# Performance work log

Measured on AMD Instinct MI355X. Metric: run time of the kernel, lower is better.

Reference implementation:

```python
import jax, jax.numpy as jnp
import numpy as np

N = 50000      # n_nodes
E = 800000     # n_edges
IN_CH = 128
HID = 128
OUT_CH = 64
N_LAYERS = 4


def _linear_params(key, fan_in, fan_out):
    kw, kb = jax.random.split(key)
    bound = 1.0 / np.sqrt(fan_in)
    W = jax.random.uniform(kw, (fan_out, fan_in), jnp.float32, -bound, bound)
    b = jax.random.uniform(kb, (fan_out,), jnp.float32, -bound, bound)
    return W, b


def setup_inputs() -> dict:
    key = jax.random.key(0)
    ks = jax.random.split(key, 5)
    x = jax.random.normal(ks[0], (N, IN_CH), jnp.float32)
    edge_index = jax.random.randint(ks[1], (2, E), 0, N, dtype=jnp.int64)
    W_in, b_in = _linear_params(ks[2], IN_CH, HID)
    conv_keys = jax.random.split(ks[3], N_LAYERS)
    Wc = jnp.stack([_linear_params(k, HID, HID)[0] for k in conv_keys])
    bc = jnp.stack([_linear_params(k, HID, HID)[1] for k in conv_keys])
    W_out, b_out = _linear_params(ks[4], HID * N_LAYERS, OUT_CH)
    return {"x": x, "edge_index": edge_index, "W_in": W_in, "b_in": b_in,
            "Wc": Wc, "bc": bc, "W_out": W_out, "b_out": b_out}


def reference(x, edge_index, W_in, b_in, Wc, bc, W_out, b_out):
    n = x.shape[0]
    # input projection + relu
    x = jax.nn.relu(x @ W_in.T + b_in)
    src, dst = edge_index[0], edge_index[1]
    loop = jnp.arange(n, dtype=edge_index.dtype)
    src_a = jnp.concatenate([src, loop])   # [E+N]
    dst_a = jnp.concatenate([dst, loop])   # [E+N]
    # symmetric-normalized degree (with self loops)
    deg = jax.ops.segment_sum(jnp.ones(src_a.shape[0], x.dtype), dst_a, num_segments=n)
    norm = (deg[src_a] * deg[dst_a]) ** -0.5
    norm = jnp.where(jnp.isinf(norm), 0.0, norm)  # guard deg==0 (original sets inf->0)
    layer_outputs = []
    for i in range(Wc.shape[0]):
        h = x @ Wc[i].T + bc[i]                     # [N, HID]
        msg = h[src_a] * norm[:, None]              # gather + scale  [E+N, HID]
        out = jax.ops.segment_sum(msg, dst_a, num_segments=n)  # scatter-add
        x = jax.nn.relu(out)
        layer_outputs.append(x)
    h = jnp.concatenate(layer_outputs, axis=-1)     # jk_mode='cat' -> [N, HID*L]
    return h @ W_out.T + b_out
```

## Files before the change

kernel.cpp:

```cpp
#include <hip/hip_runtime.h>
#include <hip/hip_bf16.h>

#ifndef MIN
#define MIN(a,b) ((a)<(b)?(a):(b))
#endif

typedef _Float16 half2_t __attribute__((ext_vector_type(2)));
typedef _Float16 half4_t __attribute__((ext_vector_type(4)));
typedef _Float16 half8_t __attribute__((ext_vector_type(8)));
typedef float floatx4 __attribute__((ext_vector_type(4)));

#define BUCKET_SHIFT 6
#define BUCKET_SIZE 64
#define SCHUNK 2048


template <int BN, int KCH, bool A_F16, bool RELU, bool BIAS, bool SCALE, bool F16OUT>
__device__ __forceinline__
void gemm_body(int bid, const void* __restrict__ Av, int lda,
               const _Float16* __restrict__ W, int ldw,
               const float* __restrict__ bias, const float* __restrict__ dinv,
               void* __restrict__ Cv, int ldc, int M) {
    constexpr int NT = BN / 16;
    __shared__ __align__(16) _Float16 Ws[BN][136];

    int tid = threadIdx.x;
    int rowBase = bid * 64;
    int w = tid >> 6;
    int lane = tid & 63;
    int lrow = lane & 15;
    int quad = lane >> 4;
    int kq = quad * 8;
    int gr = rowBase + w * 16 + lrow;

    floatx4 acc[NT];
#pragma unroll
    for (int nt = 0; nt < NT; ++nt) acc[nt] = (floatx4){0.f, 0.f, 0.f, 0.f};

#pragma unroll
    for (int kc = 0; kc < KCH; ++kc) {
#pragma unroll
        for (int i = tid; i < BN * 16; i += 256) {
            int n = i >> 4, k8 = (i & 15) * 8;
            uint4 v = *(const uint4*)(W + (size_t)n * ldw + kc * 128 + k8);
            *(uint4*)(&Ws[n][k8]) = v;
        }
        __syncthreads();

        half8_t a[4];
        if (gr < M) {
            if (A_F16) {
                const _Float16* A = (const _Float16*)Av;
                const _Float16* ap = A + (size_t)gr * lda + kc * 128 + kq;
#pragma unroll
                for (int ks = 0; ks < 4; ++ks)
                    a[ks] = *(const half8_t*)(ap + ks * 32);
            } else {
                const float* A = (const float*)Av;
                const float* ap = A + (size_t)gr * lda + kc * 128 + kq;
#pragma unroll
                for (int ks = 0; ks < 4; ++ks) {
                    float4 v0 = *(const float4*)(ap + ks * 32);
                    float4 v1 = *(const float4*)(ap + ks * 32 + 4);
                    half8_t h;
                    h[0] = (_Float16)v0.x; h[1] = (_Float16)v0.y;
                    h[2] = (_Float16)v0.z; h[3] = (_Float16)v0.w;
                    h[4] = (_Float16)v1.x; h[5] = (_Float16)v1.y;
                    h[6] = (_Float16)v1.z; h[7] = (_Float16)v1.w;
                    a[ks] = h;
                }
            }
        } else {
#pragma unroll
            for (int ks = 0; ks < 4; ++ks)
                a[ks] = (half8_t){0, 0, 0, 0, 0, 0, 0, 0};
        }

#pragma unroll
        for (int ks = 0; ks < 4; ++ks) {
            int kk = ks * 32 + kq;
#pragma unroll
            for (int nt = 0; nt < NT; ++nt) {
                half8_t b = *(const half8_t*)(&Ws[nt * 16 + lrow][kk]);
                acc[nt] = __builtin_amdgcn_mfma_f32_16x16x32_f16(a[ks], b, acc[nt], 0, 0, 0);
            }
        }
        if (kc != KCH - 1) __syncthreads();
    }

#pragma unroll
    for (int nt = 0; nt < NT; ++nt) {
        int col = nt * 16 + lrow;
        float bv = BIAS ? bias[col] : 0.0f;
#pragma unroll
        for (int reg = 0; reg < 4; ++reg) {
            int gr2 = rowBase + w * 16 + quad * 4 + reg;
            if (gr2 < M) {
                float v = acc[nt][reg] + bv;
                if (RELU) v = fmaxf(v, 0.0f);
                if (SCALE) v *= dinv[gr2];
                if (F16OUT) {
                    _Float16* C = (_Float16*)Cv;
                    C[(size_t)gr2 * ldc + col] = (_Float16)v;
                } else {
                    float* C = (float*)Cv;
                    C[(size_t)gr2 * ldc + col] = v;
                }
            }
        }
    }
}

template <int BN, int KCH, bool A_F16, bool RELU, bool BIAS, bool SCALE, bool F16OUT>
__global__ __launch_bounds__(256)
void mfma_gemm(const void* __restrict__ Av, int lda,
               const _Float16* __restrict__ W, int ldw,
               const float* __restrict__ bias, const float* __restrict__ dinv,
               void* __restrict__ Cv, int ldc, int M) {
    gemm_body<BN, KCH, A_F16, RELU, BIAS, SCALE, F16OUT>(
        blockIdx.x, Av, lda, W, ldw, bias, dinv, Cv, ldc, M);
}


__global__ __launch_bounds__(256)
void k_hist_cvt(const int* __restrict__ dst, int E, int* __restrict__ bucketCnt, int NB,
                const float* __restrict__ a, _Float16* __restrict__ oa, int na,
                const float* __restrict__ b, _Float16* __restrict__ ob, int nb,
                const float* __restrict__ c, _Float16* __restrict__ oc, int nc,
                _Float16* __restrict__ zrow) {
    __shared__ int h[1024];
    int t = threadIdx.x;
    if (blockIdx.x < 512) {
        for (int i = t; i < 1024; i += 256) h[i] = 0;
        __syncthreads();
        for (int e = blockIdx.x * 256 + t; e < E; e += 512 * 256)
            atomicAdd(&h[dst[e] >> BUCKET_SHIFT], 1);
        __syncthreads();
        for (int i = t; i < NB; i += 256)
            if (h[i]) atomicAdd(&bucketCnt[i], h[i]);
    } else {
        int i = (blockIdx.x - 512) * 256 + t;
        if (i < na) oa[i] = (_Float16)a[i];
        if (i < nb) ob[i] = (_Float16)b[i];
        if (i < nc) oc[i] = (_Float16)c[i];
        if (i < 128) zrow[i] = (_Float16)0.0f;
    }
}

__global__ void bucket_scan(const int* __restrict__ bucketCnt,
                            int* __restrict__ bucketBase, int* __restrict__ bucketCur,
                            int NB, int E) {
    __shared__ int sm[1024];
    int t = threadIdx.x;
    int v = (t < NB) ? bucketCnt[t] : 0;
    sm[t] = v;
    __syncthreads();
    for (int off = 1; off < 1024; off <<= 1) {
        int add = (t >= off) ? sm[t - off] : 0;
        __syncthreads();
        sm[t] += add;
        __syncthreads();
    }
    if (t < NB) {
        bucketBase[t] = sm[t] - v;
        bucketCur[t] = sm[t] - v;
    }
    if (t == 0) bucketBase[NB] = E;
}


__global__ __launch_bounds__(256)
void k_scatter_proj(const int* __restrict__ src, const int* __restrict__ dst, int E,
                    int* __restrict__ bucketCur, unsigned int* __restrict__ rec, int SB,
                    const float* __restrict__ A, const _Float16* __restrict__ W,
                    const float* __restrict__ bias, _Float16* __restrict__ Cout, int M) {
    __shared__ int hist[1024];
    __shared__ int base[1024];
    if (blockIdx.x < SB) {
        int t = threadIdx.x;
        int e0 = blockIdx.x * SCHUNK;
        int e1 = MIN(E, e0 + SCHUNK);
        for (int i = t; i < 1024; i += 256) hist[i] = 0;
        __syncthreads();
        for (int e = e0 + t; e < e1; e += 256)
            atomicAdd(&hist[dst[e] >> BUCKET_SHIFT], 1);
        __syncthreads();
        for (int i = t; i < 1024; i += 256) {
            int c = hist[i];
            base[i] = c ? atomicAdd(&bucketCur[i], c) : 0;
            hist[i] = 0;
        }
        __syncthreads();
        for (int e = e0 + t; e < e1; e += 256) {
            int d = dst[e];
            int bk = d >> BUCKET_SHIFT;
            int pos = base[bk] + atomicAdd(&hist[bk], 1);
            rec[pos] = (unsigned)src[e] | ((unsigned)(d & (BUCKET_SIZE - 1)) << 16);
        }
    } else {
        gemm_body<128, 1, false, true, true, false, true>(
            blockIdx.x - SB, A, 128, W, 128, bias, nullptr, Cout, 128, M);
    }
}

__global__ void bucket_build(const unsigned int* __restrict__ rec,
                             const int* __restrict__ bucketBase,
                             int* __restrict__ rowptr, unsigned short* __restrict__ csr_src,
                             float* __restrict__ dinv, int N, int E) {
    __shared__ int lcnt[256];
    __shared__ int sm[256];
    __shared__ int lcur[64];
    int b = blockIdx.x;
    int t = threadIdx.x;
    int beg = bucketBase[b], end = bucketBase[b + 1];
    lcnt[t] = 0;
    __syncthreads();
    for (int i = beg + t; i < end; i += 256)
        atomicAdd(&lcnt[rec[i] >> 16], 1);
    __syncthreads();
    int v = lcnt[t];
    sm[t] = v;
    __syncthreads();
    for (int off = 1; off < 256; off <<= 1) {
        int add = (t >= off) ? sm[t - off] : 0;
        __syncthreads();
        sm[t] += add;
        __syncthreads();
    }
    int excl = sm[t] - v;
    if (t < BUCKET_SIZE) {
        int node = b * BUCKET_SIZE + t;
        if (node < N) {
            rowptr[node] = beg + excl;
            dinv[node] = rsqrtf((float)(v + 1));
        }
        lcur[t] = beg + excl;
    }
    __syncthreads();
    for (int i = beg + t; i < end; i += 256) {
        unsigned int r = rec[i];
        int pos = atomicAdd(&lcur[r >> 16], 1);
        csr_src[pos] = (unsigned short)(r & 0xFFFFu);
    }
    if (b == 0 && t == 0) rowptr[N] = E;
}


__global__ __launch_bounds__(256)
void agg_kernel(const half2_t* __restrict__ Hb, const float* __restrict__ dinv,
                const int* __restrict__ rowptr,
                const unsigned short* __restrict__ csr_src,
                half2_t* __restrict__ X, int N) {
    int node = blockIdx.x * 4 + (threadIdx.x >> 6);
    int t = threadIdx.x & 63;
    if (node >= N) return;
    float di = dinv[node];
    half2_t hu = Hb[(size_t)node * 64 + t];
    float2 acc;
    acc.x = (float)hu.x;
    acc.y = (float)hu.y;
    int beg = rowptr[node];
    int end = rowptr[node + 1];

    for (int base = beg; base < end; base += 64) {
        int idx = base + t;
        int s_lane = (idx < end) ? (int)csr_src[idx] : N;
        int m = end - base;
        if (m > 64) m = 64;
        int mm = (m + 15) & ~15;
        for (int j = 0; j < mm; j += 16) {
            int s[16];
#pragma unroll
            for (int k = 0; k < 16; ++k) s[k] = __shfl(s_lane, j + k);
            half2_t u[16];
#pragma unroll
            for (int k = 0; k < 16; ++k) u[k] = Hb[(size_t)s[k] * 64 + t];
#pragma unroll
            for (int k = 0; k < 16; ++k) {
                acc.x += (float)u[k].x;
                acc.y += (float)u[k].y;
            }
        }
    }
    half2_t o;
    o.x = (_Float16)fmaxf(acc.x * di, 0.0f);
    o.y = (_Float16)fmaxf(acc.y * di, 0.0f);
    X[(size_t)node * 256 + t] = o;
}


extern "C" void kernel_launch(void* const* d_in, const int* in_sizes, int n_in,
                              void* d_out, int out_size, void* d_ws, size_t ws_size,
                              hipStream_t stream) {
    const float* x     = (const float*)d_in[0];
    const int*   ei    = (const int*)d_in[1];
    const float* W_in  = (const float*)d_in[2];
    const float* b_in  = (const float*)d_in[3];
    const float* Wc    = (const float*)d_in[4];
    const float* bc    = (const float*)d_in[5];
    const float* W_out = (const float*)d_in[6];
    const float* b_out = (const float*)d_in[7];
    float* out = (float*)d_out;

    const int HID = 128;
    const int N = in_sizes[0] / HID;
    const int E = in_sizes[1] / 2;
    const int L = 4;
    const int* src = ei;
    const int* dst = ei + E;
    const int NB = (N + BUCKET_SIZE - 1) >> BUCKET_SHIFT;

    char* ws = (char*)d_ws;
    size_t off = 0;
    auto carve = [&](size_t bytes) {
        void* p = ws + off;
        off += (bytes + 255) & ~(size_t)255;
        return p;
    };
    float* dinv        = (float*)carve((size_t)N * 4);
    int*   rowptr      = (int*)carve((size_t)(N + 1) * 4);
    unsigned short* csr_src = (unsigned short*)carve((size_t)E * 2);
    unsigned int* rec  = (unsigned int*)carve((size_t)E * 4);
    int*   bucketCnt   = (int*)carve((size_t)1024 * 4);
    int*   bucketBase  = (int*)carve((size_t)1025 * 4);
    int*   bucketCur   = (int*)carve((size_t)1024 * 4);
    _Float16* bufA     = (_Float16*)carve((size_t)N * HID * 2);
    _Float16* bufH     = (_Float16*)carve((size_t)(N + 1) * HID * 2);
    _Float16* bufXcat  = (_Float16*)carve((size_t)N * 512 * 2);
    _Float16* Wf_in    = (_Float16*)carve((size_t)HID * HID * 2);
    _Float16* Wf_c     = (_Float16*)carve((size_t)L * HID * HID * 2);
    _Float16* Wf_out   = (_Float16*)carve((size_t)64 * 512 * 2);
    (void)ws_size;

    int gemm_blocks = (N + 63) / 64;
    int SB = (E + SCHUNK - 1) / SCHUNK;

    hipMemsetAsync(bucketCnt, 0, (size_t)1024 * 4, stream);
    k_hist_cvt<<<512 + 256, 256, 0, stream>>>(
        dst, E, bucketCnt, NB,
        W_in, Wf_in, HID * HID,
        Wc, Wf_c, L * HID * HID,
        W_out, Wf_out, 64 * 512,
        bufH + (size_t)N * HID);
    bucket_scan<<<1, 1024, 0, stream>>>(bucketCnt, bucketBase, bucketCur, NB, E);
    k_scatter_proj<<<SB + gemm_blocks, 256, 0, stream>>>(
        src, dst, E, bucketCur, rec, SB,
        x, Wf_in, b_in, bufA, N);
    bucket_build<<<NB, 256, 0, stream>>>(rec, bucketBase, rowptr, csr_src, dinv, N, E);

    for (int l = 0; l < L; ++l) {
        const void* Ain = (l == 0) ? (const void*)bufA
                                   : (const void*)(bufXcat + (size_t)(l - 1) * 128);
        int lda = (l == 0) ? 128 : 512;
        mfma_gemm<128, 1, true, false, true, true, true>
            <<<gemm_blocks, 256, 0, stream>>>(Ain, lda, Wf_c + (size_t)l * HID * HID, HID,
                                              bc + (size_t)l * HID, dinv, bufH, HID, N);
        agg_kernel<<<(N + 3) / 4, 256, 0, stream>>>((const half2_t*)bufH, dinv, rowptr,
                                                    csr_src,
                                                    (half2_t*)bufXcat + (size_t)l * 64, N);
    }

    mfma_gemm<64, 4, true, false, true, false, false>
        <<<gemm_blocks, 256, 0, stream>>>(bufXcat, 512, Wf_out, 512, b_out, nullptr,
                                          out, 64, N);
}
```

Before: 320.7 us.

## Gather neighbor rows with 16-byte loads across four lane groups in aggregation

The aggregation kernel now splits each 64-lane wavefront into four groups of 16 lanes. Each group loads a whole 256-byte neighbor row using uint4 (8 fp16) loads, so every iteration handles 16 neighbors with 4 wide loads per lane instead of 16 narrow half2 loads. Partial sums are combined across groups with xor shuffles, and one group writes the result with a single vector store. This cuts the number of load instructions and raises the bytes fetched per request, at the cost of more registers for accumulators and extra cross-lane reduction.

```diff
diff --git a/kernel.cpp b/kernel.cpp
--- a/kernel.cpp
+++ b/kernel.cpp
@@ -247,45 +247,69 @@
 
 
 __global__ __launch_bounds__(256)
-void agg_kernel(const half2_t* __restrict__ Hb, const float* __restrict__ dinv,
+void agg_kernel(const uint4* __restrict__ Hb4, const float* __restrict__ dinv,
                 const int* __restrict__ rowptr,
                 const unsigned short* __restrict__ csr_src,
-                half2_t* __restrict__ X, int N) {
+                _Float16* __restrict__ X, int N) {
     int node = blockIdx.x * 4 + (threadIdx.x >> 6);
     int t = threadIdx.x & 63;
     if (node >= N) return;
+    int g = t >> 4;
+    int c = t & 15;
     float di = dinv[node];
-    half2_t hu = Hb[(size_t)node * 64 + t];
-    float2 acc;
-    acc.x = (float)hu.x;
-    acc.y = (float)hu.y;
     int beg = rowptr[node];
     int end = rowptr[node + 1];
+
+    float acc[8] = {0.f, 0.f, 0.f, 0.f, 0.f, 0.f, 0.f, 0.f};
+
+    {
+        int selfs = (g == 0) ? node : N;
+        uint4 su = Hb4[(size_t)selfs * 16 + c];
+        half8_t h = *(const half8_t*)&su;
+#pragma unroll
+        for (int i = 0; i < 8; ++i) acc[i] += (float)h[i];
+    }
 
     for (int base = beg; base < end; base += 64) {
         int idx = base + t;
         int s_lane = (idx < end) ? (int)csr_src[idx] : N;
         int m = end - base;
         if (m > 64) m = 64;
-        int mm = (m + 15) & ~15;
-        for (int j = 0; j < mm; j += 16) {
-            int s[16];
-#pragma unroll
-            for (int k = 0; k < 16; ++k) s[k] = __shfl(s_lane, j + k);
-            half2_t u[16];
-#pragma unroll
-            for (int k = 0; k < 16; ++k) u[k] = Hb[(size_t)s[k] * 64 + t];
-#pragma unroll
-            for (int k = 0; k < 16; ++k) {
-                acc.x += (float)u[k].x;
-                acc.y += (float)u[k].y;
+        for (int j = 0; j < m; j += 16) {
+            int s0 = __shfl(s_lane, j + g);
+            int s1 = __shfl(s_lane, j + 4 + g);
+            int s2 = __shfl(s_lane, j + 8 + g);
+            int s3 = __shfl(s_lane, j + 12 + g);
+            uint4 u0 = Hb4[(size_t)s0 * 16 + c];
+            uint4 u1 = Hb4[(size_t)s1 * 16 + c];
+            uint4 u2 = Hb4[(size_t)s2 * 16 + c];
+            uint4 u3 = Hb4[(size_t)s3 * 16 + c];
+            half8_t h0 = *(const half8_t*)&u0;
+            half8_t h1 = *(const half8_t*)&u1;
+            half8_t h2 = *(const half8_t*)&u2;
+            half8_t h3 = *(const half8_t*)&u3;
+#pragma unroll
+            for (int i = 0; i < 8; ++i) {
+                acc[i] += (float)h0[i];
+                acc[i] += (float)h1[i];
+                acc[i] += (float)h2[i];
+                acc[i] += (float)h3[i];
             }
         }
     }
-    half2_t o;
-    o.x = (_Float16)fmaxf(acc.x * di, 0.0f);
-    o.y = (_Float16)fmaxf(acc.y * di, 0.0f);
-    X[(size_t)node * 256 + t] = o;
+
+#pragma unroll
+    for (int i = 0; i < 8; ++i) {
+        acc[i] += __shfl_xor(acc[i], 16);
+        acc[i] += __shfl_xor(acc[i], 32);
+    }
+
+    if (g == 0) {
+        half8_t o;
+#pragma unroll
+        for (int i = 0; i < 8; ++i) o[i] = (_Float16)fmaxf(acc[i] * di, 0.0f);
+        *(half8_t*)(X + (size_t)node * 512 + c * 8) = o;
+    }
 }
 
 
@@ -355,9 +379,9 @@
         mfma_gemm<128, 1, true, false, true, true, true>
             <<<gemm_blocks, 256, 0, stream>>>(Ain, lda, Wf_c + (size_t)l * HID * HID, HID,
                                               bc + (size_t)l * HID, dinv, bufH, HID, N);
-        agg_kernel<<<(N + 3) / 4, 256, 0, stream>>>((const half2_t*)bufH, dinv, rowptr,
+        agg_kernel<<<(N + 3) / 4, 256, 0, stream>>>((const uint4*)bufH, dinv, rowptr,
                                                     csr_src,
-                                                    (half2_t*)bufXcat + (size_t)l * 64, N);
+                                                    bufXcat + (size_t)l * 128, N);
     }
 
     mfma_gemm<64, 4, true, false, true, false, false>
```

After: 323.1 us. About the same (+0.7%).

## Split CSR into source-residue segments and aggregate several nodes per wave

Applied to the files above, without the earlier changes.

The CSR build now sorts each destination's edges into 4 sub-segments keyed by the low two bits of the source index, and stores a per-(node, segment) row pointer. The aggregation kernel gives each wave 7 consecutive nodes and walks all nodes segment by segment, using a fixed grid of 2048 blocks and gather batches of 8 instead of 16. The intent is better temporal locality of the feature gathers across the waves running at the same time. In exchange, each node's short edge list is cut into smaller pieces that are padded to 8, which adds wasted loads of the zero row. There are also fewer waves in flight and more serial work per wave.

```diff
diff --git a/kernel.cpp b/kernel.cpp
--- a/kernel.cpp
+++ b/kernel.cpp
@@ -13,6 +13,9 @@
 #define BUCKET_SHIFT 6
 #define BUCKET_SIZE 64
 #define SCHUNK 2048
+#define NSEG 4
+#define SEGMASK 3
+#define NPW 7
 
 
 template <int BN, int KCH, bool A_F16, bool RELU, bool BIAS, bool SCALE, bool F16OUT>
@@ -203,20 +206,23 @@
     }
 }
 
+
 __global__ void bucket_build(const unsigned int* __restrict__ rec,
                              const int* __restrict__ bucketBase,
-                             int* __restrict__ rowptr, unsigned short* __restrict__ csr_src,
+                             int* __restrict__ rowptr2, unsigned short* __restrict__ csr_src,
                              float* __restrict__ dinv, int N, int E) {
     __shared__ int lcnt[256];
     __shared__ int sm[256];
-    __shared__ int lcur[64];
+    __shared__ int lcur[256];
     int b = blockIdx.x;
     int t = threadIdx.x;
     int beg = bucketBase[b], end = bucketBase[b + 1];
     lcnt[t] = 0;
     __syncthreads();
-    for (int i = beg + t; i < end; i += 256)
-        atomicAdd(&lcnt[rec[i] >> 16], 1);
+    for (int i = beg + t; i < end; i += 256) {
+        unsigned int r = rec[i];
+        atomicAdd(&lcnt[((r >> 16) & 63) * NSEG + (r & SEGMASK)], 1);
+    }
     __syncthreads();
     int v = lcnt[t];
     sm[t] = v;
@@ -228,64 +234,99 @@
         __syncthreads();
     }
     int excl = sm[t] - v;
+    rowptr2[b * 256 + t] = beg + excl;
+    lcur[t] = beg + excl;
     if (t < BUCKET_SIZE) {
         int node = b * BUCKET_SIZE + t;
         if (node < N) {
-            rowptr[node] = beg + excl;
-            dinv[node] = rsqrtf((float)(v + 1));
-        }
-        lcur[t] = beg + excl;
+            int deg = lcnt[t * 4] + lcnt[t * 4 + 1] + lcnt[t * 4 + 2] + lcnt[t * 4 + 3];
+            dinv[node] = rsqrtf((float)(deg + 1));
+        }
     }
     __syncthreads();
     for (int i = beg + t; i < end; i += 256) {
         unsigned int r = rec[i];
-        int pos = atomicAdd(&lcur[r >> 16], 1);
+        int pos = atomicAdd(&lcur[((r >> 16) & 63) * NSEG + (r & SEGMASK)], 1);
         csr_src[pos] = (unsigned short)(r & 0xFFFFu);
     }
-    if (b == 0 && t == 0) rowptr[N] = E;
+    if (b == 0 && t == 0) rowptr2[gridDim.x * 256] = E;
 }
 
 
 __global__ __launch_bounds__(256)
 void agg_kernel(const half2_t* __restrict__ Hb, const float* __restrict__ dinv,
-                const int* __restrict__ rowptr,
+                const int* __restrict__ rowptr2,
                 const unsigned short* __restrict__ csr_src,
                 half2_t* __restrict__ X, int N) {
-    int node = blockIdx.x * 4 + (threadIdx.x >> 6);
+    int wid = blockIdx.x * 4 + (threadIdx.x >> 6);
     int t = threadIdx.x & 63;
-    if (node >= N) return;
-    float di = dinv[node];
-    half2_t hu = Hb[(size_t)node * 64 + t];
-    float2 acc;
-    acc.x = (float)hu.x;
-    acc.y = (float)hu.y;
-    int beg = rowptr[node];
-    int end = rowptr[node + 1];
-
-    for (int base = beg; base < end; base += 64) {
-        int idx = base + t;
-        int s_lane = (idx < end) ? (int)csr_src[idx] : N;
-        int m = end - base;
-        if (m > 64) m = 64;
-        int mm = (m + 15) & ~15;
-        for (int j = 0; j < mm; j += 16) {
-            int s[16];
-#pragma unroll
-            for (int k = 0; k < 16; ++k) s[k] = __shfl(s_lane, j + k);
-            half2_t u[16];
-#pragma unroll
-            for (int k = 0; k < 16; ++k) u[k] = Hb[(size_t)s[k] * 64 + t];
-#pragma unroll
-            for (int k = 0; k < 16; ++k) {
-                acc.x += (float)u[k].x;
-                acc.y += (float)u[k].y;
+    int n0 = wid * NPW;
+
+    float2 acc[NPW];
+    float di[NPW];
+#pragma unroll
+    for (int n = 0; n < NPW; ++n) {
+        int node = n0 + n;
+        if (node < N) {
+            di[n] = dinv[node];
+            half2_t hu = Hb[(size_t)node * 64 + t];
+            acc[n].x = (float)hu.x;
+            acc[n].y = (float)hu.y;
+        } else {
+            di[n] = 0.0f;
+            acc[n].x = 0.0f;
+            acc[n].y = 0.0f;
+        }
+    }
+
+    for (int s = 0; s < NSEG; ++s) {
+#pragma unroll
+        for (int n = 0; n < NPW; ++n) {
+            int node = n0 + n;
+            if (node >= N) continue;
+            int beg = rowptr2[node * NSEG + s];
+            int end = rowptr2[node * NSEG + s + 1];
+            for (int base = beg; base < end; base += 64) {
+                int idx = base + t;
+                int s_lane = (idx < end) ? (int)csr_src[idx] : N;
+                int m = end - base;
+                if (m > 64) m = 64;
+                int mm = (m + 7) & ~7;
+                for (int j = 0; j < mm; j += 8) {
+                    int s0 = __shfl(s_lane, j + 0), s1 = __shfl(s_lane, j + 1);
+                    int s2 = __shfl(s_lane, j + 2), s3 = __shfl(s_lane, j + 3);
+                    int s4 = __shfl(s_lane, j + 4), s5 = __shfl(s_lane, j + 5);
+                    int s6 = __shfl(s_lane, j + 6), s7 = __shfl(s_lane, j + 7);
+                    half2_t u0 = Hb[(size_t)s0 * 64 + t];
+                    half2_t u1 = Hb[(size_t)s1 * 64 + t];
+                    half2_t u2 = Hb[(size_t)s2 * 64 + t];
+                    half2_t u3 = Hb[(size_t)s3 * 64 + t];
+                    half2_t u4 = Hb[(size_t)s4 * 64 + t];
+                    half2_t u5 = Hb[(size_t)s5 * 64 + t];
+                    half2_t u6 = Hb[(size_t)s6 * 64 + t];
+                    half2_t u7 = Hb[(size_t)s7 * 64 + t];
+                    acc[n].x += (float)u0.x; acc[n].y += (float)u0.y;
+                    acc[n].x += (float)u1.x; acc[n].y += (float)u1.y;
+                    acc[n].x += (float)u2.x; acc[n].y += (float)u2.y;
+                    acc[n].x += (float)u3.x; acc[n].y += (float)u3.y;
+                    acc[n].x += (float)u4.x; acc[n].y += (float)u4.y;
+                    acc[n].x += (float)u5.x; acc[n].y += (float)u5.y;
+                    acc[n].x += (float)u6.x; acc[n].y += (float)u6.y;
+                    acc[n].x += (float)u7.x; acc[n].y += (float)u7.y;
+                }
             }
         }
     }
-    half2_t o;
-    o.x = (_Float16)fmaxf(acc.x * di, 0.0f);
-    o.y = (_Float16)fmaxf(acc.y * di, 0.0f);
-    X[(size_t)node * 256 + t] = o;
+
+#pragma unroll
+    for (int n = 0; n < NPW; ++n) {
+        int node = n0 + n;
+        if (node >= N) continue;
+        half2_t o;
+        o.x = (_Float16)fmaxf(acc[n].x * di[n], 0.0f);
+        o.y = (_Float16)fmaxf(acc[n].y * di[n], 0.0f);
+        X[(size_t)node * 256 + t] = o;
+    }
 }
 
 
@@ -318,7 +359,7 @@
         return p;
     };
     float* dinv        = (float*)carve((size_t)N * 4);
-    int*   rowptr      = (int*)carve((size_t)(N + 1) * 4);
+    int*   rowptr2     = (int*)carve(((size_t)NB * 256 + 8) * 4);
     unsigned short* csr_src = (unsigned short*)carve((size_t)E * 2);
     unsigned int* rec  = (unsigned int*)carve((size_t)E * 4);
     int*   bucketCnt   = (int*)carve((size_t)1024 * 4);
@@ -334,6 +375,7 @@
 
     int gemm_blocks = (N + 63) / 64;
     int SB = (E + SCHUNK - 1) / SCHUNK;
+    int agg_blocks = 2048;
 
     hipMemsetAsync(bucketCnt, 0, (size_t)1024 * 4, stream);
     k_hist_cvt<<<512 + 256, 256, 0, stream>>>(
@@ -346,7 +388,7 @@
     k_scatter_proj<<<SB + gemm_blocks, 256, 0, stream>>>(
         src, dst, E, bucketCur, rec, SB,
         x, Wf_in, b_in, bufA, N);
-    bucket_build<<<NB, 256, 0, stream>>>(rec, bucketBase, rowptr, csr_src, dinv, N, E);
+    bucket_build<<<NB, 256, 0, stream>>>(rec, bucketBase, rowptr2, csr_src, dinv, N, E);
 
     for (int l = 0; l < L; ++l) {
         const void* Ain = (l == 0) ? (const void*)bufA
@@ -355,9 +397,9 @@
         mfma_gemm<128, 1, true, false, true, true, true>
             <<<gemm_blocks, 256, 0, stream>>>(Ain, lda, Wf_c + (size_t)l * HID * HID, HID,
                                               bc + (size_t)l * HID, dinv, bufH, HID, N);
-        agg_kernel<<<(N + 3) / 4, 256, 0, stream>>>((const half2_t*)bufH, dinv, rowptr,
-                                                    csr_src,
-                                                    (half2_t*)bufXcat + (size_t)l * 64, N);
+        agg_kernel<<<agg_blocks, 256, 0, stream>>>((const half2_t*)bufH, dinv, rowptr2,
+                                                   csr_src,
+                                                   (half2_t*)bufXcat + (size_t)l * 64, N);
     }
 
     mfma_gemm<64, 4, true, false, true, false, false>
```

Measured after the change: 386.4 us. +20.5%, slower.

## Fuse neighbor aggregation with following layer GEMM and output projection

Applied to the files above, without the earlier changes.

Each layer's gather-aggregation is merged with the next layer's 128x128 MFMA projection in one kernel. The aggregated rows are staged in LDS as the GEMM A operand, with ping-pong H buffers between layers. The final layer's aggregation is fused into the output projection, so layer 4 is never written to Xcat and the earlier slabs are read from global memory. This removes four kernel launches and one round-trip of layer outputs, but cuts parallelism from 12.5k blocks of 4 nodes to about 782 blocks of 64 nodes, so each wave aggregates 16 nodes serially and the gather loses latency hiding.

```diff
diff --git a/kernel.cpp b/kernel.cpp
--- a/kernel.cpp
+++ b/kernel.cpp
@@ -122,12 +122,198 @@
 }
 
 
+__device__ __forceinline__
+float2 agg_node(const half2_t* __restrict__ Hin, const int* __restrict__ rowptr,
+                const unsigned short* __restrict__ csr_src, int node, int lane, int N) {
+    half2_t hu = Hin[(size_t)node * 64 + lane];
+    float2 acc;
+    acc.x = (float)hu.x;
+    acc.y = (float)hu.y;
+    int beg = rowptr[node];
+    int end = rowptr[node + 1];
+    for (int base = beg; base < end; base += 64) {
+        int idx = base + lane;
+        int s_lane = (idx < end) ? (int)csr_src[idx] : N;
+        int m = end - base;
+        if (m > 64) m = 64;
+        int mm = (m + 15) & ~15;
+        for (int j = 0; j < mm; j += 16) {
+            int s[16];
+#pragma unroll
+            for (int k = 0; k < 16; ++k) s[k] = __shfl(s_lane, j + k);
+            half2_t u[16];
+#pragma unroll
+            for (int k = 0; k < 16; ++k) u[k] = Hin[(size_t)s[k] * 64 + lane];
+#pragma unroll
+            for (int k = 0; k < 16; ++k) {
+                acc.x += (float)u[k].x;
+                acc.y += (float)u[k].y;
+            }
+        }
+    }
+    return acc;
+}
+
+
+__global__ __launch_bounds__(256)
+void fused_agg_conv(const half2_t* __restrict__ Hin, const float* __restrict__ dinv,
+                    const int* __restrict__ rowptr,
+                    const unsigned short* __restrict__ csr_src,
+                    half2_t* __restrict__ Xslab,
+                    const _Float16* __restrict__ W,
+                    const float* __restrict__ bias,
+                    _Float16* __restrict__ Hout, int N) {
+    __shared__ __align__(16) _Float16 As[64][136];
+    __shared__ __align__(16) _Float16 Ws[128][136];
+    int tid = threadIdx.x;
+    int w = tid >> 6;
+    int lane = tid & 63;
+    int rowBase = blockIdx.x * 64;
+
+#pragma unroll
+    for (int i = tid; i < 128 * 16; i += 256) {
+        int n = i >> 4, k8 = (i & 15) * 8;
+        *(uint4*)(&Ws[n][k8]) = *(const uint4*)(W + (size_t)n * 128 + k8);
+    }
+
+    for (int nn = 0; nn < 16; ++nn) {
+        int node = rowBase + w * 16 + nn;
+        half2_t o = {(_Float16)0.0f, (_Float16)0.0f};
+        if (node < N) {
+            float di = dinv[node];
+            float2 acc = agg_node(Hin, rowptr, csr_src, node, lane, N);
+            o.x = (_Float16)fmaxf(acc.x * di, 0.0f);
+            o.y = (_Float16)fmaxf(acc.y * di, 0.0f);
+            Xslab[(size_t)node * 256 + lane] = o;
+        }
+        *(half2_t*)(&As[w * 16 + nn][lane * 2]) = o;
+    }
+    __syncthreads();
+
+    int lrow = lane & 15;
+    int quad = lane >> 4;
+    int kq = quad * 8;
+    floatx4 acc[8];
+#pragma unroll
+    for (int nt = 0; nt < 8; ++nt) acc[nt] = (floatx4){0.f, 0.f, 0.f, 0.f};
+#pragma unroll
+    for (int ks = 0; ks < 4; ++ks) {
+        int kk = ks * 32 + kq;
+        half8_t a = *(const half8_t*)(&As[w * 16 + lrow][kk]);
+#pragma unroll
+        for (int nt = 0; nt < 8; ++nt) {
+            half8_t b = *(const half8_t*)(&Ws[nt * 16 + lrow][kk]);
+            acc[nt] = __builtin_amdgcn_mfma_f32_16x16x32_f16(a, b, acc[nt], 0, 0, 0);
+        }
+    }
+#pragma unroll
+    for (int nt = 0; nt < 8; ++nt) {
+        int col = nt * 16 + lrow;
+        float bv = bias[col];
+#pragma unroll
+        for (int reg = 0; reg < 4; ++reg) {
+            int gr2 = rowBase + w * 16 + quad * 4 + reg;
+            if (gr2 < N) {
+                float v = (acc[nt][reg] + bv) * dinv[gr2];
+                Hout[(size_t)gr2 * 128 + col] = (_Float16)v;
+            }
+        }
+    }
+}
+
+
+__global__ __launch_bounds__(256)
+void fused_agg_out(const half2_t* __restrict__ Hin, const float* __restrict__ dinv,
+                   const int* __restrict__ rowptr,
+                   const unsigned short* __restrict__ csr_src,
+                   const _Float16* __restrict__ Xcat,
+                   const _Float16* __restrict__ W,
+                   const float* __restrict__ bias, float* __restrict__ out, int N) {
+    __shared__ __align__(16) _Float16 As[64][136];
+    __shared__ __align__(16) _Float16 Ws[64][136];
+    int tid = threadIdx.x;
+    int w = tid >> 6;
+    int lane = tid & 63;
+    int rowBase = blockIdx.x * 64;
+
+    for (int nn = 0; nn < 16; ++nn) {
+        int node = rowBase + w * 16 + nn;
+        half2_t o = {(_Float16)0.0f, (_Float16)0.0f};
+        if (node < N) {
+            float di = dinv[node];
+            float2 acc = agg_node(Hin, rowptr, csr_src, node, lane, N);
+            o.x = (_Float16)fmaxf(acc.x * di, 0.0f);
+            o.y = (_Float16)fmaxf(acc.y * di, 0.0f);
+        }
+        *(half2_t*)(&As[w * 16 + nn][lane * 2]) = o;
+    }
+
+    int lrow = lane & 15;
+    int quad = lane >> 4;
+    int kq = quad * 8;
+    int gr = rowBase + w * 16 + lrow;
+
+    floatx4 acc[4];
+#pragma unroll
+    for (int nt = 0; nt < 4; ++nt) acc[nt] = (floatx4){0.f, 0.f, 0.f, 0.f};
+
+#pragma unroll
+    for (int kc = 0; kc < 4; ++kc) {
+        __syncthreads();
+#pragma unroll
+        for (int i = tid; i < 64 * 16; i += 256) {
+            int n = i >> 4, k8 = (i & 15) * 8;
+            *(uint4*)(&Ws[n][k8]) = *(const uint4*)(W + (size_t)n * 512 + kc * 128 + k8);
+        }
+        __syncthreads();
+
+        half8_t a[4];
+        if (kc == 3) {
+#pragma unroll
+            for (int ks = 0; ks < 4; ++ks)
+                a[ks] = *(const half8_t*)(&As[w * 16 + lrow][ks * 32 + kq]);
+        } else if (gr < N) {
+            const _Float16* ap = Xcat + (size_t)gr * 512 + kc * 128 + kq;
+#pragma unroll
+            for (int ks = 0; ks < 4; ++ks)
+                a[ks] = *(const half8_t*)(ap + ks * 32);
+        } else {
+#pragma unroll
+            for (int ks = 0; ks < 4; ++ks)
+                a[ks] = (half8_t){0, 0, 0, 0, 0, 0, 0, 0};
+        }
+
+#pragma unroll
+        for (int ks = 0; ks < 4; ++ks) {
+            int kk = ks * 32 + kq;
+#pragma unroll
+            for (int nt = 0; nt < 4; ++nt) {
+                half8_t b = *(const half8_t*)(&Ws[nt * 16 + lrow][kk]);
+                acc[nt] = __builtin_amdgcn_mfma_f32_16x16x32_f16(a[ks], b, acc[nt], 0, 0, 0);
+            }
+        }
+    }
+
+#pragma unroll
+    for (int nt = 0; nt < 4; ++nt) {
+        int col = nt * 16 + lrow;
+        float bv = bias[col];
+#pragma unroll
+        for (int reg = 0; reg < 4; ++reg) {
+            int gr2 = rowBase + w * 16 + quad * 4 + reg;
+            if (gr2 < N)
+                out[(size_t)gr2 * 64 + col] = acc[nt][reg] + bv;
+        }
+    }
+}
+
+
 __global__ __launch_bounds__(256)
 void k_hist_cvt(const int* __restrict__ dst, int E, int* __restrict__ bucketCnt, int NB,
                 const float* __restrict__ a, _Float16* __restrict__ oa, int na,
                 const float* __restrict__ b, _Float16* __restrict__ ob, int nb,
                 const float* __restrict__ c, _Float16* __restrict__ oc, int nc,
-                _Float16* __restrict__ zrow) {
+                _Float16* __restrict__ zrow1, _Float16* __restrict__ zrow2) {
     __shared__ int h[1024];
     int t = threadIdx.x;
     if (blockIdx.x < 512) {
@@ -143,7 +329,7 @@
         if (i < na) oa[i] = (_Float16)a[i];
         if (i < nb) ob[i] = (_Float16)b[i];
         if (i < nc) oc[i] = (_Float16)c[i];
-        if (i < 128) zrow[i] = (_Float16)0.0f;
+        if (i < 128) { zrow1[i] = (_Float16)0.0f; zrow2[i] = (_Float16)0.0f; }
     }
 }
 
@@ -246,49 +432,6 @@
 }
 
 
-__global__ __launch_bounds__(256)
-void agg_kernel(const half2_t* __restrict__ Hb, const float* __restrict__ dinv,
-                const int* __restrict__ rowptr,
-                const unsigned short* __restrict__ csr_src,
-                half2_t* __restrict__ X, int N) {
-    int node = blockIdx.x * 4 + (threadIdx.x >> 6);
-    int t = threadIdx.x & 63;
-    if (node >= N) return;
-    float di = dinv[node];
-    half2_t hu = Hb[(size_t)node * 64 + t];
-    float2 acc;
-    acc.x = (float)hu.x;
-    acc.y = (float)hu.y;
-    int beg = rowptr[node];
-    int end = rowptr[node + 1];
-
-    for (int base = beg; base < end; base += 64) {
-        int idx = base + t;
-        int s_lane = (idx < end) ? (int)csr_src[idx] : N;
-        int m = end - base;
-        if (m > 64) m = 64;
-        int mm = (m + 15) & ~15;
-        for (int j = 0; j < mm; j += 16) {
-            int s[16];
-#pragma unroll
-            for (int k = 0; k < 16; ++k) s[k] = __shfl(s_lane, j + k);
-            half2_t u[16];
-#pragma unroll
-            for (int k = 0; k < 16; ++k) u[k] = Hb[(size_t)s[k] * 64 + t];
-#pragma unroll
-            for (int k = 0; k < 16; ++k) {
-                acc.x += (float)u[k].x;
-                acc.y += (float)u[k].y;
-            }
-        }
-    }
-    half2_t o;
-    o.x = (_Float16)fmaxf(acc.x * di, 0.0f);
-    o.y = (_Float16)fmaxf(acc.y * di, 0.0f);
-    X[(size_t)node * 256 + t] = o;
-}
-
-
 extern "C" void kernel_launch(void* const* d_in, const int* in_sizes, int n_in,
                               void* d_out, int out_size, void* d_ws, size_t ws_size,
                               hipStream_t stream) {
@@ -325,7 +468,8 @@
     int*   bucketBase  = (int*)carve((size_t)1025 * 4);
     int*   bucketCur   = (int*)carve((size_t)1024 * 4);
     _Float16* bufA     = (_Float16*)carve((size_t)N * HID * 2);
-    _Float16* bufH     = (_Float16*)carve((size_t)(N + 1) * HID * 2);
+    _Float16* bufHa    = (_Float16*)carve((size_t)(N + 1) * HID * 2);
+    _Float16* bufHb    = (_Float16*)carve((size_t)(N + 1) * HID * 2);
     _Float16* bufXcat  = (_Float16*)carve((size_t)N * 512 * 2);
     _Float16* Wf_in    = (_Float16*)carve((size_t)HID * HID * 2);
     _Float16* Wf_c     = (_Float16*)carve((size_t)L * HID * HID * 2);
@@ -341,26 +485,27 @@
         W_in, Wf_in, HID * HID,
         Wc, Wf_c, L * HID * HID,
         W_out, Wf_out, 64 * 512,
-        bufH + (size_t)N * HID);
+        bufHa + (size_t)N * HID, bufHb + (size_t)N * HID);
     bucket_scan<<<1, 1024, 0, stream>>>(bucketCnt, bucketBase, bucketCur, NB, E);
     k_scatter_proj<<<SB + gemm_blocks, 256, 0, stream>>>(
         src, dst, E, bucketCur, rec, SB,
         x, Wf_in, b_in, bufA, N);
     bucket_build<<<NB, 256, 0, stream>>>(rec, bucketBase, rowptr, csr_src, dinv, N, E);
 
-    for (int l = 0; l < L; ++l) {
-        const void* Ain = (l == 0) ? (const void*)bufA
-                                   : (const void*)(bufXcat + (size_t)(l - 1) * 128);
-        int lda = (l == 0) ? 128 : 512;
-        mfma_gemm<128, 1, true, false, true, true, true>
-            <<<gemm_blocks, 256, 0, stream>>>(Ain, lda, Wf_c + (size_t)l * HID * HID, HID,
-                                              bc + (size_t)l * HID, dinv, bufH, HID, N);
-        agg_kernel<<<(N + 3) / 4, 256, 0, stream>>>((const half2_t*)bufH, dinv, rowptr,
-                                                    csr_src,
-                                                    (half2_t*)bufXcat + (size_t)l * 64, N);
-    }
-
-    mfma_gemm<64, 4, true, false, true, false, false>
-        <<<gemm_blocks, 256, 0, stream>>>(bufXcat, 512, Wf_out, 512, b_out, nullptr,
-                                          out, 64, N);
-}
+    mfma_gemm<128, 1, true, false, true, true, true>
+        <<<gemm_blocks, 256, 0, stream>>>(bufA, 128, Wf_c, HID, bc, dinv, bufHa, HID, N);
+
+    fused_agg_conv<<<gemm_blocks, 256, 0, stream>>>(
+        (const half2_t*)bufHa, dinv, rowptr, csr_src,
+        (half2_t*)bufXcat + 0 * 64, Wf_c + 1 * HID * HID, bc + 1 * HID, bufHb, N);
+    fused_agg_conv<<<gemm_blocks, 256, 0, stream>>>(
+        (const half2_t*)bufHb, dinv, rowptr, csr_src,
+        (half2_t*)bufXcat + 1 * 64, Wf_c + 2 * HID * HID, bc + 2 * HID, bufHa, N);
+    fused_agg_conv<<<gemm_blocks, 256, 0, stream>>>(
+        (const half2_t*)bufHa, dinv, rowptr, csr_src,
+        (half2_t*)bufXcat + 2 * 64, Wf_c + 3 * HID * HID, bc + 3 * HID, bufHb, N);
+
+    fused_agg_out<<<gemm_blocks, 256, 0, stream>>>(
+        (const half2_t*)bufHb, dinv, rowptr, csr_src,
+        bufXcat, Wf_out, b_out, out, N);
+}
```

After: 406.2 us. 26.7% more time.
